# Kernel optimization log

Measured on AMD Instinct MI355X. Metric: run time of the kernel, lower is better.

Reference implementation:

```python
import jax, jax.numpy as jnp
import numpy as np

B, T, H, V = 256, 256, 512, 32000
L = 3  # stacked LSTM layers


def setup_inputs() -> dict:
    key = jax.random.key(0)
    ks = jax.random.split(key, 12)
    s = 0.05
    n = lambda k, shp: (jax.random.normal(k, shp, jnp.float32) * s)
    return {
        "text_1": jax.random.randint(ks[0], (B, T), 0, V, dtype=jnp.int32),
        "text_2": jax.random.randint(ks[1], (B, T), 0, V, dtype=jnp.int32),
        "text_3": jax.random.randint(ks[2], (B, T), 0, V, dtype=jnp.int32),
        "emb": n(ks[3], (V, H)),
        "Wx": n(ks[4], (L, H, 4 * H)),
        "Wh": n(ks[5], (L, H, 4 * H)),
        "b": jnp.zeros((L, 4 * H), jnp.float32),
        "g1": jnp.ones((3 * H,), jnp.float32), "beta1": jnp.zeros((3 * H,), jnp.float32),
        "W1": n(ks[6], (3 * H, 2 * H)), "bd1": jnp.zeros((2 * H,), jnp.float32),
        "g2": jnp.ones((2 * H,), jnp.float32), "beta2": jnp.zeros((2 * H,), jnp.float32),
        "W2": n(ks[7], (2 * H, H // 5)), "bd2": jnp.zeros((H // 5,), jnp.float32),
        "g3": jnp.ones((H // 5,), jnp.float32), "beta3": jnp.zeros((H // 5,), jnp.float32),
        "W3": n(ks[8], (H // 5, 4)), "bd3": jnp.zeros((4,), jnp.float32),
    }


def _lstm_stack(tokens, emb, Wx, Wh, b):
    # tokens: [B, T] int -> last hidden of top layer [B, H]
    x = emb[tokens]                      # [B, T, H]
    x = jnp.transpose(x, (1, 0, 2))      # [T, B, H] (scan over time)
    bsz, h = x.shape[1], Wh.shape[1]
    for l in range(Wx.shape[0]):
        Wx_l, Wh_l, b_l = Wx[l], Wh[l], b[l]
        def step(carry, xt):
            hprev, cprev = carry
            gates = xt @ Wx_l + hprev @ Wh_l + b_l      # [B, 4H]
            i, f, g, o = jnp.split(gates, 4, axis=-1)
            c = jax.nn.sigmoid(f) * cprev + jax.nn.sigmoid(i) * jnp.tanh(g)
            hnew = jax.nn.sigmoid(o) * jnp.tanh(c)
            return (hnew, c), hnew
        init = (jnp.zeros((bsz, h), x.dtype), jnp.zeros((bsz, h), x.dtype))
        _, x = jax.lax.scan(step, init, x)
    return x[-1]                          # rnn_output[:, -1, :]


def _bn(x, gamma, beta, eps=1e-3):
    m = jnp.mean(x, axis=0)
    v = jnp.var(x, axis=0)
    return gamma * (x - m) * jax.lax.rsqrt(v + eps) + beta


def reference(text_1, text_2, text_3, emb, Wx, Wh, b,
              g1, beta1, W1, bd1, g2, beta2, W2, bd2, g3, beta3, W3, bd3):
    r1 = _lstm_stack(text_1, emb, Wx, Wh, b)
    r2 = _lstm_stack(text_2, emb, Wx, Wh, b)
    r3 = _lstm_stack(text_3, emb, Wx, Wh, b)
    r = jnp.concatenate([r1, r2, r3], axis=1)   # [B, 3H]
    r = _bn(r, g1, beta1)
    r = jax.nn.selu(r @ W1 + bd1)
    r = _bn(r, g2, beta2)
    r = jax.nn.selu(r @ W2 + bd2)
    r = _bn(r, g3, beta3)
    return r @ W3 + bd3                          # [B, 4] logits
```

## Files before the change

kernel.cpp:

```cpp
#include <hip/hip_runtime.h>
#include <hip/hip_bf16.h>
#include <hip/hip_cooperative_groups.h>

namespace cg = cooperative_groups;

typedef __attribute__((ext_vector_type(8))) short short8;
typedef __attribute__((ext_vector_type(4))) float floatx4;

namespace {
constexpr int kB1 = 256;
constexpr int kT  = 256;
constexpr int kH  = 512;
constexpr int kL  = 3;
constexpr int kK  = 1024;
constexpr int kN  = 2048;
constexpr int kGrid = 576;
constexpr size_t kHB = (size_t)768 * kH;

constexpr size_t WREP_OFF   = 0;
constexpr size_t WREP_BYTES = (size_t)kL * kK * kN * 2;
constexpr size_t BREP_OFF   = WREP_OFF + WREP_BYTES;
constexpr size_t BREP_BYTES = (size_t)kL * kN * 4;
constexpr size_t HBUF_OFF   = BREP_OFF + BREP_BYTES;
constexpr size_t HBUF_BYTES = (size_t)kL * 2 * kHB * 2;
constexpr size_t CBUF_OFF   = HBUF_OFF + HBUF_BYTES;
constexpr size_t CBUF_BYTES = (size_t)kL * kHB * 4;
constexpr size_t BNA_OFF    = CBUF_OFF + CBUF_BYTES;
constexpr size_t BNC_OFF    = BNA_OFF + 1536 * 4;
constexpr size_t Z1_OFF     = BNC_OFF + 1536 * 4;
constexpr size_t Z2_OFF     = Z1_OFF + (size_t)256 * 1024 * 4;
constexpr size_t FLAG_OFF   = Z2_OFF + (size_t)256 * 102 * 4;
}

__device__ __forceinline__ float ldf(const void* p, size_t idx, int isf32) {
  if (isf32) return ((const float*)p)[idx];
  return __bfloat162float(((const __hip_bfloat16*)p)[idx]);
}

__device__ __forceinline__ short f2bs(float x) {
  union { __hip_bfloat16 h; short s; } u;
  u.h = __float2bfloat16(x);
  return u.s;
}

__device__ __forceinline__ void sync_lds() {
  asm volatile("s_waitcnt lgkmcnt(0)\n\ts_barrier" ::: "memory");
}

__device__ __forceinline__ float fast_tanh(float x) {
  float e = __expf(2.f * x);
  return __fdividef(e - 1.f, e + 1.f);
}
__device__ __forceinline__ float fast_sigmoid(float x) {
  return __fdividef(1.f, 1.f + __expf(-x));
}

__global__ void detect_kernel(const unsigned* __restrict__ g1, int* __restrict__ flag) {
  if (threadIdx.x == 0 && blockIdx.x == 0)
    *flag = (g1[0] == 0x3F800000u) ? 1 : 0;
}

__device__ __forceinline__ void repack_body(
    int start, int stride,
    const void* __restrict__ Wx, const void* __restrict__ Wh,
    const void* __restrict__ bias, int isf32,
    __hip_bfloat16* __restrict__ Wrep, float* __restrict__ brep) {
  for (int idx = start; idx < kL * kK * kN; idx += stride) {
    int j  = idx & 7;
    int n2 = (idx >> 3) & (kN - 1);
    int kg = (idx >> 14) & 127;
    int l  = idx >> 21;
    int k  = kg * 8 + j;
    int ntile = n2 >> 7, c = n2 & 127, g = c >> 5, ul = c & 31;
    int u = ntile * 32 + ul;
    int col = g * 512 + u;
    float v;
    if (k < kH) v = ldf(Wx, ((size_t)l * kH + k) * kN + col, isf32);
    else        v = ldf(Wh, ((size_t)l * kH + (k - kH)) * kN + col, isf32);
    Wrep[idx] = __float2bfloat16(v);
    if (kg == 0 && j == 0) brep[l * kN + n2] = ldf(bias, (size_t)l * kN + col, isf32);
  }
}

__global__ __launch_bounds__(256) void repack_kernel(
    const void* __restrict__ Wx, const void* __restrict__ Wh,
    const void* __restrict__ bias, const int* __restrict__ flagp,
    __hip_bfloat16* __restrict__ Wrep, float* __restrict__ brep) {
  repack_body(blockIdx.x * 256 + threadIdx.x, gridDim.x * 256, Wx, Wh, bias, *flagp,
              Wrep, brep);
}

__device__ __forceinline__ void lstm_step(
    int l, int mt, int nt, int t, int isf32,
    const __hip_bfloat16* __restrict__ WB, float bv0, float bv1,
    __hip_bfloat16* __restrict__ hbuf, float* __restrict__ cl,
    const void* __restrict__ emb, const int* __restrict__ txt,
    char* smem) {
  const int tid = threadIdx.x;
  const int lane = tid & 63;
  const int lm = lane & 15, lq = lane >> 4;
  const int arow = tid >> 2;
  const int kc   = tid & 3;
  const int row_g = mt * 64 + arow;
  const int n0w = nt * 128 + (tid >> 6) * 32;

  const void* xsrc;  bool xf32 = false;
  if (l == 0) {
    int tok = txt[t];
    if (isf32) { xsrc = (const void*)((const float*)emb + (size_t)tok * kH); xf32 = true; }
    else         xsrc = (const void*)((const __hip_bfloat16*)emb + (size_t)tok * kH);
  } else {
    const __hip_bfloat16* hIn = hbuf + ((size_t)(l - 1) * 2 + (t & 1)) * kHB;
    xsrc = (const void*)(hIn + (size_t)row_g * kH);
  }
  const __hip_bfloat16* hrow = nullptr;
  if (t > 0) {
    const __hip_bfloat16* hPrev = hbuf + ((size_t)l * 2 + ((t & 1) ^ 1)) * kHB;
    hrow = hPrev + (size_t)row_g * kH;
  }

  const int e_uu = tid & 31;
  const int e_r0 = tid >> 5;

  char* const buf0 = smem;
  char* const buf1 = smem + 16384;
  const int abase = ((arow >> 4) * 256 + kc * 16 + (arow & 15)) * 16;

  short8 av[4];
  short8 bf[4][2];

  auto loadA = [&](int sl) {
    if ((sl >= 4) && (t == 0)) {
      short8 vz = {0, 0, 0, 0, 0, 0, 0, 0};
#pragma unroll
      for (int jj = 0; jj < 4; jj++) av[jj] = vz;
    } else if (sl < 4 && xf32) {
      const float* sf = (const float*)xsrc + sl * 128;
#pragma unroll
      for (int jj = 0; jj < 4; jj++) {
        const float* q = sf + kc * 8 + jj * 32;
        float4 lo = *(const float4*)q;
        float4 hi = *(const float4*)(q + 4);
        short8 v;
        v[0] = f2bs(lo.x); v[1] = f2bs(lo.y); v[2] = f2bs(lo.z); v[3] = f2bs(lo.w);
        v[4] = f2bs(hi.x); v[5] = f2bs(hi.y); v[6] = f2bs(hi.z); v[7] = f2bs(hi.w);
        av[jj] = v;
      }
    } else {
      const __hip_bfloat16* src = (sl < 4)
          ? ((const __hip_bfloat16*)xsrc + sl * 128)
          : (hrow + (sl - 4) * 128);
#pragma unroll
      for (int jj = 0; jj < 4; jj++)
        av[jj] = *(const short8*)(src + kc * 8 + jj * 32);
    }
  };
  auto writeA = [&](char* b) {
#pragma unroll
    for (int jj = 0; jj < 4; jj++)
      *(short8*)(b + abase + jj * 1024) = av[jj];
  };
  auto loadBfrag = [&](int sl, int kk) {
#pragma unroll
    for (int nf = 0; nf < 2; nf++) {
      size_t kg = (size_t)(sl * 16 + kk * 4 + lq);
      bf[kk][nf] = *(const short8*)(WB + (kg * kN + (n0w + nf * 16 + lm)) * 8);
    }
  };

  loadA(0);
#pragma unroll
  for (int kk = 0; kk < 4; kk++) loadBfrag(0, kk);
  writeA(buf0);
  loadA(1);
  float cold[8];
  if (t > 0) {
#pragma unroll
    for (int ii = 0; ii < 8; ii++) {
      int rowf = e_r0 + 8 * ii;
      cold[ii] = cl[(size_t)(mt * 64 + rowf) * kH + nt * 32 + e_uu];
    }
  } else {
#pragma unroll
    for (int ii = 0; ii < 8; ii++) cold[ii] = 0.f;
  }
  sync_lds();

  floatx4 zf = {0.f, 0.f, 0.f, 0.f};
  floatx4 acc[4][2];
#pragma unroll
  for (int a = 0; a < 4; a++)
#pragma unroll
    for (int b = 0; b < 2; b++) acc[a][b] = zf;

#pragma unroll 1
  for (int sl = 0; sl < 8; sl++) {
    char* const cur = (sl & 1) ? buf1 : buf0;
    char* const nxt = (sl & 1) ? buf0 : buf1;
    if (sl < 7) writeA(nxt);
    if (sl < 6) loadA(sl + 2);
#pragma unroll
    for (int kk = 0; kk < 4; kk++) {
      short8 afrag[4];
#pragma unroll
      for (int mf = 0; mf < 4; mf++)
        afrag[mf] = *(const short8*)(cur + (mf * 4 + kk) * 1024 + lane * 16);
#pragma unroll
      for (int mf = 0; mf < 4; mf++)
#pragma unroll
        for (int nf = 0; nf < 2; nf++)
          acc[mf][nf] = __builtin_amdgcn_mfma_f32_16x16x32_bf16(
              afrag[mf], bf[kk][nf], acc[mf][nf], 0, 0, 0);
      if (sl < 7) loadBfrag(sl + 1, kk);
    }
    sync_lds();
  }

#pragma unroll
  for (int mf = 0; mf < 4; mf++)
#pragma unroll
    for (int r = 0; r < 4; r++) {
      acc[mf][0][r] += bv0;
      acc[mf][1][r] += bv1;
    }

  float* gl = (float*)smem;
  {
    const int wv = tid >> 6;
#pragma unroll
    for (int mf = 0; mf < 4; mf++)
#pragma unroll
      for (int nf = 0; nf < 2; nf++)
#pragma unroll
        for (int r = 0; r < 4; r++) {
          int rowf = mf * 16 + lq * 4 + r;
          int uu   = nf * 16 + lm;
          gl[((size_t)wv * 64 + rowf) * 34 + uu] = acc[mf][nf][r];
        }
  }
  sync_lds();

  __hip_bfloat16* hout = hbuf + ((size_t)l * 2 + (t & 1)) * kHB;
#pragma unroll
  for (int ii = 0; ii < 8; ii++) {
    int rowf = e_r0 + 8 * ii;
    int uu = e_uu;
    float gi = fminf(fmaxf(gl[(0 * 64 + rowf) * 34 + uu], -40.f), 40.f);
    float gf = fminf(fmaxf(gl[(1 * 64 + rowf) * 34 + uu], -40.f), 40.f);
    float gG = fminf(fmaxf(gl[(2 * 64 + rowf) * 34 + uu], -40.f), 40.f);
    float go = fminf(fmaxf(gl[(3 * 64 + rowf) * 34 + uu], -40.f), 40.f);
    size_t off = (size_t)(mt * 64 + rowf) * kH + nt * 32 + uu;
    float cn = fast_sigmoid(gf) * cold[ii] + fast_sigmoid(gi) * fast_tanh(gG);
    float hn = fast_sigmoid(go) * fast_tanh(cn);
    cl[off] = cn;
    hout[off] = __float2bfloat16(hn);
  }
  sync_lds();
}

__global__ __launch_bounds__(256, 3) void persist_kernel(
    const void* __restrict__ Wx, const void* __restrict__ Wh,
    const void* __restrict__ bias, const int* __restrict__ flagp,
    __hip_bfloat16* __restrict__ Wrep, float* __restrict__ brep,
    __hip_bfloat16* __restrict__ hbuf, float* __restrict__ cbuf,
    const void* __restrict__ emb,
    const int* __restrict__ t1, const int* __restrict__ t2, const int* __restrict__ t3) {
  cg::grid_group gg = cg::this_grid();
  __shared__ __align__(16) char smem[34816];

  const int bid = blockIdx.x;
  const int tid = threadIdx.x;
  const int isf32 = *flagp;

  repack_body(bid * 256 + tid, kGrid * 256, Wx, Wh, bias, isf32, Wrep, brep);
  gg.sync();

  const int l  = bid / 192;
  const int rr = bid % 192;
  const int nt = rr & 15;
  const int mt = rr >> 4;
  const __hip_bfloat16* const WB = Wrep + (size_t)l * kK * kN;
  float* const cl = cbuf + (size_t)l * kHB;
  const int n0w = nt * 128 + (tid >> 6) * 32;
  const int lm = tid & 15;
  const float bv0 = brep[l * kN + n0w + lm];
  const float bv1 = brep[l * kN + n0w + 16 + lm];

  const int* txt = nullptr;
  if (l == 0) {
    int row_g = mt * 64 + (tid >> 2);
    int i = row_g >> 8;
    txt = (i == 0) ? t1 : (i == 1) ? t2 : t3;
    txt += (row_g & 255) * kT;
  }

  for (int s = 0; s < kT + kL - 1; s++) {
    const int t = s - l;
    if (t >= 0 && t < kT)
      lstm_step(l, mt, nt, t, isf32, WB, bv0, bv1, hbuf, cl, emb, txt, smem);
    gg.sync();
  }
}

__global__ __launch_bounds__(256, 3) void step_kernel(
    int s,
    const __hip_bfloat16* __restrict__ Wrep, const float* __restrict__ brep,
    __hip_bfloat16* __restrict__ hbuf, float* __restrict__ cbuf,
    const void* __restrict__ emb, const int* __restrict__ flagp,
    const int* __restrict__ t1, const int* __restrict__ t2, const int* __restrict__ t3) {
  __shared__ __align__(16) char smem[34816];
  const int bid = blockIdx.x;
  const int l  = bid / 192;
  const int rr = bid % 192;
  const int nt = rr & 15;
  const int mt = rr >> 4;
  const int t = s - l;
  if (t < 0 || t >= kT) return;
  const int isf32 = *flagp;
  const int tid = threadIdx.x;
  const __hip_bfloat16* WB = Wrep + (size_t)l * kK * kN;
  float* cl = cbuf + (size_t)l * kHB;
  const int n0w = nt * 128 + (tid >> 6) * 32;
  const int lm = tid & 15;
  const float bv0 = brep[l * kN + n0w + lm];
  const float bv1 = brep[l * kN + n0w + 16 + lm];
  const int* txt = nullptr;
  if (l == 0) {
    int row_g = mt * 64 + (tid >> 2);
    int i = row_g >> 8;
    txt = (i == 0) ? t1 : (i == 1) ? t2 : t3;
    txt += (row_g & 255) * kT;
  }
  lstm_step(l, mt, nt, t, isf32, WB, bv0, bv1, hbuf, cl, emb, txt, smem);
}

__global__ __launch_bounds__(256) void stats_kernel(
    int ncols, int mode, const void* __restrict__ src,
    const void* __restrict__ gamma, const void* __restrict__ beta,
    const int* __restrict__ flagp, float* __restrict__ bn_a, float* __restrict__ bn_c) {
  int isf32 = *flagp;
  int col = blockIdx.x * 256 + threadIdx.x;
  if (col >= ncols) return;
  float sum = 0.f, ss = 0.f;
  for (int b = 0; b < kB1; b++) {
    float v;
    if (mode == 0) {
      const __hip_bfloat16* h = (const __hip_bfloat16*)src;
      v = __bfloat162float(h[((size_t)((col >> 9) * kB1 + b)) * kH + (col & 511)]);
    } else {
      v = ((const float*)src)[(size_t)b * ncols + col];
    }
    v = fmaxf(-1e15f, fminf(v, 1e15f));
    sum += v; ss += v * v;
  }
  float mean = sum * (1.f / kB1);
  float var  = ss * (1.f / kB1) - mean * mean;
  float a = ldf(gamma, col, isf32) * rsqrtf(var + 1e-3f);
  bn_a[col] = a;
  bn_c[col] = ldf(beta, col, isf32) - mean * a;
}

__global__ __launch_bounds__(256) void headgemm_kernel(
    int Kd, int Nd, int mode, const void* __restrict__ Asrc,
    const float* __restrict__ bn_a, const float* __restrict__ bn_c,
    const void* __restrict__ W, const void* __restrict__ bias,
    const int* __restrict__ flagp, float* __restrict__ out, int do_selu) {
  __shared__ float As[32][65];
  __shared__ float Bs[32][65];
  int isf32 = *flagp;
  int tid = threadIdx.x;
  int bx = blockIdx.x, by = blockIdx.y;
  int tx = tid & 15, ty = tid >> 4;
  float acc[4][4] = {};
  int am = tid & 63, ak = tid >> 6;
  int bk = tid >> 3, bn8 = (tid & 7) * 8;
  for (int ks = 0; ks < Kd; ks += 32) {
    __syncthreads();
    for (int jj = 0; jj < 8; jj++) {
      int kl = ak * 8 + jj;
      int kg = ks + kl;
      int mg = by * 64 + am;
      float v;
      if (mode == 0) {
        const __hip_bfloat16* h = (const __hip_bfloat16*)Asrc;
        v = __bfloat162float(h[((size_t)((kg >> 9) * kB1 + mg)) * kH + (kg & 511)]);
      } else {
        v = ((const float*)Asrc)[(size_t)mg * Kd + kg];
      }
      As[kl][am] = v * bn_a[kg] + bn_c[kg];
    }
    for (int e = 0; e < 8; e++) {
      int col = bx * 64 + bn8 + e;
      Bs[bk][bn8 + e] = (col < Nd) ? ldf(W, (size_t)(ks + bk) * Nd + col, isf32) : 0.f;
    }
    __syncthreads();
    for (int k = 0; k < 32; k++) {
      float ar[4], br[4];
#pragma unroll
      for (int i = 0; i < 4; i++) ar[i] = As[k][ty * 4 + i];
#pragma unroll
      for (int j = 0; j < 4; j++) br[j] = Bs[k][tx * 4 + j];
#pragma unroll
      for (int i = 0; i < 4; i++)
#pragma unroll
        for (int j = 0; j < 4; j++) acc[i][j] += ar[i] * br[j];
    }
  }
  for (int i = 0; i < 4; i++) {
    int row = by * 64 + ty * 4 + i;
    for (int j = 0; j < 4; j++) {
      int col = bx * 64 + tx * 4 + j;
      if (col < Nd) {
        float y = acc[i][j] + ldf(bias, col, isf32);
        if (do_selu)
          y = (y > 0.f) ? 1.0507009873554805f * y
                        : 1.0507009873554805f * 1.6732632423543772f * (__expf(y) - 1.f);
        out[(size_t)row * Nd + col] = y;
      }
    }
  }
}

__global__ __launch_bounds__(256) void final_kernel(
    const float* __restrict__ z2, const float* __restrict__ bn_a, const float* __restrict__ bn_c,
    const void* __restrict__ W3, const void* __restrict__ bd3,
    const int* __restrict__ flagp, void* __restrict__ out) {
  int isf32 = *flagp;
  int b = threadIdx.x;
  float acc[4] = {0.f, 0.f, 0.f, 0.f};
  for (int j = 0; j < 102; j++) {
    float y = z2[b * 102 + j] * bn_a[j] + bn_c[j];
#pragma unroll
    for (int g = 0; g < 4; g++) acc[g] += y * ldf(W3, j * 4 + g, isf32);
  }
#pragma unroll
  for (int g = 0; g < 4; g++) {
    float y = acc[g] + ldf(bd3, g, isf32);
    if (isf32) ((float*)out)[b * 4 + g] = y;
    else ((__hip_bfloat16*)out)[b * 4 + g] = __float2bfloat16(y);
  }
}

extern "C" void kernel_launch(void* const* d_in, const int* in_sizes, int n_in,
                              void* d_out, int out_size, void* d_ws, size_t ws_size,
                              hipStream_t stream) {
  const int* t1 = (const int*)d_in[0];
  const int* t2 = (const int*)d_in[1];
  const int* t3 = (const int*)d_in[2];
  const void* emb = d_in[3];
  const void* Wx  = d_in[4];
  const void* Wh  = d_in[5];
  const void* bb  = d_in[6];
  const void* g1  = d_in[7];
  const void* be1 = d_in[8];
  const void* W1  = d_in[9];
  const void* bd1 = d_in[10];
  const void* g2  = d_in[11];
  const void* be2 = d_in[12];
  const void* W2  = d_in[13];
  const void* bd2 = d_in[14];
  const void* g3  = d_in[15];
  const void* be3 = d_in[16];
  const void* W3  = d_in[17];
  const void* bd3 = d_in[18];

  char* ws = (char*)d_ws;
  __hip_bfloat16* Wrep = (__hip_bfloat16*)(ws + WREP_OFF);
  float* brep = (float*)(ws + BREP_OFF);
  __hip_bfloat16* hbuf = (__hip_bfloat16*)(ws + HBUF_OFF);
  float* cbuf = (float*)(ws + CBUF_OFF);
  float* bn_a = (float*)(ws + BNA_OFF);
  float* bn_c = (float*)(ws + BNC_OFF);
  float* z1 = (float*)(ws + Z1_OFF);
  float* z2 = (float*)(ws + Z2_OFF);
  int* flag = (int*)(ws + FLAG_OFF);

  detect_kernel<<<1, 64, 0, stream>>>((const unsigned*)g1, flag);

  bool coop_ok = false;
  {
    int numCU = 0, maxBlk = 0;
    int dev = 0;
    if (hipGetDevice(&dev) == hipSuccess &&
        hipDeviceGetAttribute(&numCU, hipDeviceAttributeMultiprocessorCount, dev) == hipSuccess &&
        hipOccupancyMaxActiveBlocksPerMultiprocessor(&maxBlk, (const void*)persist_kernel,
                                                     256, 0) == hipSuccess) {
      if ((long)maxBlk * numCU >= kGrid) {
        void* args[] = {(void*)&Wx, (void*)&Wh, (void*)&bb, (void*)&flag,
                        (void*)&Wrep, (void*)&brep, (void*)&hbuf, (void*)&cbuf,
                        (void*)&emb, (void*)&t1, (void*)&t2, (void*)&t3};
        hipError_t err = hipLaunchCooperativeKernel((const void*)persist_kernel,
                                                    dim3(kGrid), dim3(256), args, 0, stream);
        if (err == hipSuccess) coop_ok = true;
        else (void)hipGetLastError();
      }
    } else {
      (void)hipGetLastError();
    }
  }
  if (!coop_ok) {
    repack_kernel<<<(kL * kK * kN) / 256, 256, 0, stream>>>(Wx, Wh, bb, flag, Wrep, brep);
    for (int s = 0; s < kT + kL - 1; s++)
      step_kernel<<<kGrid, 256, 0, stream>>>(s, Wrep, brep, hbuf, cbuf, emb, flag, t1, t2, t3);
  }

  const __hip_bfloat16* hTop = hbuf + (2 * 2 + 1) * kHB;
  stats_kernel<<<6, 256, 0, stream>>>(1536, 0, hTop, g1, be1, flag, bn_a, bn_c);
  headgemm_kernel<<<dim3(16, 4), 256, 0, stream>>>(1536, 1024, 0, hTop, bn_a, bn_c, W1, bd1, flag, z1, 1);
  stats_kernel<<<4, 256, 0, stream>>>(1024, 1, z1, g2, be2, flag, bn_a, bn_c);
  headgemm_kernel<<<dim3(2, 4), 256, 0, stream>>>(1024, 102, 1, z1, bn_a, bn_c, W2, bd2, flag, z2, 1);
  stats_kernel<<<1, 256, 0, stream>>>(102, 1, z2, g3, be3, flag, bn_a, bn_c);
  final_kernel<<<1, 256, 0, stream>>>(z2, bn_a, bn_c, W3, bd3, flag, (void*)d_out);
}
```

Before: 6.522 ms.

## Replace grid-wide sync with per-row-tile atomic barriers and XCD-aware tile mapping

Replaces the cooperative-groups grid.sync after each timestep with custom atomic barriers scoped to the 48 blocks that share an M row-tile across all layers and N tiles. Blocks claim work slots through per-XCD atomic counters so that N tiles land on a chosen XCD, which is meant to improve L2 locality of the weight slices. The aim is to cut the cost of 258 full-grid barriers down to smaller group barriers. The trailing LDS sync in the step is dropped and the sync counters are zeroed in the detect kernel. The correctness risk lies in the cross-layer dependencies between groups and in the memory ordering of the hand-written spin barrier.

```diff
diff --git a/kernel.cpp b/kernel.cpp
--- a/kernel.cpp
+++ b/kernel.cpp
@@ -1,8 +1,5 @@
 #include <hip/hip_runtime.h>
 #include <hip/hip_bf16.h>
-#include <hip/hip_cooperative_groups.h>
-
-namespace cg = cooperative_groups;
 
 typedef __attribute__((ext_vector_type(8))) short short8;
 typedef __attribute__((ext_vector_type(4))) float floatx4;
@@ -29,7 +26,8 @@
 constexpr size_t BNC_OFF    = BNA_OFF + 1536 * 4;
 constexpr size_t Z1_OFF     = BNC_OFF + 1536 * 4;
 constexpr size_t Z2_OFF     = Z1_OFF + (size_t)256 * 1024 * 4;
-constexpr size_t FLAG_OFF   = Z2_OFF + (size_t)256 * 102 * 4;
+constexpr size_t SYNC_OFF   = Z2_OFF + (size_t)256 * 102 * 4;
+constexpr int kSyncUints = 32 * 14;
 }
 
 __device__ __forceinline__ float ldf(const void* p, size_t idx, int isf32) {
@@ -47,6 +45,25 @@
   asm volatile("s_waitcnt lgkmcnt(0)\n\ts_barrier" ::: "memory");
 }
 
+__device__ __forceinline__ void gbar(unsigned* line, unsigned target, unsigned want) {
+  __syncthreads();
+  if (threadIdx.x == 0) {
+    __threadfence();
+    unsigned old = __hip_atomic_fetch_add(&line[0], 1u, __ATOMIC_ACQ_REL,
+                                          __HIP_MEMORY_SCOPE_AGENT);
+    if (old == target - 1) {
+      __hip_atomic_store(&line[0], 0u, __ATOMIC_RELAXED, __HIP_MEMORY_SCOPE_AGENT);
+      __hip_atomic_store(&line[1], want, __ATOMIC_RELEASE, __HIP_MEMORY_SCOPE_AGENT);
+    } else {
+      while (__hip_atomic_load(&line[1], __ATOMIC_ACQUIRE,
+                               __HIP_MEMORY_SCOPE_AGENT) < want)
+        __builtin_amdgcn_s_sleep(1);
+    }
+    __threadfence();
+  }
+  __syncthreads();
+}
+
 __device__ __forceinline__ float fast_tanh(float x) {
   float e = __expf(2.f * x);
   return __fdividef(e - 1.f, e + 1.f);
@@ -55,9 +72,10 @@
   return __fdividef(1.f, 1.f + __expf(-x));
 }
 
-__global__ void detect_kernel(const unsigned* __restrict__ g1, int* __restrict__ flag) {
-  if (threadIdx.x == 0 && blockIdx.x == 0)
-    *flag = (g1[0] == 0x3F800000u) ? 1 : 0;
+__global__ void detect_kernel(const unsigned* __restrict__ g1, unsigned* __restrict__ sync) {
+  int i = threadIdx.x;
+  for (int j = i; j < kSyncUints; j += 256) sync[j] = 0u;
+  if (i == 0) sync[0] = (g1[0] == 0x3F800000u) ? 1u : 0u;
 }
 
 __device__ __forceinline__ void repack_body(
@@ -255,30 +273,48 @@
     cl[off] = cn;
     hout[off] = __float2bfloat16(hn);
   }
-  sync_lds();
 }
 
 __global__ __launch_bounds__(256, 3) void persist_kernel(
     const void* __restrict__ Wx, const void* __restrict__ Wh,
-    const void* __restrict__ bias, const int* __restrict__ flagp,
+    const void* __restrict__ bias, unsigned* __restrict__ sync,
     __hip_bfloat16* __restrict__ Wrep, float* __restrict__ brep,
     __hip_bfloat16* __restrict__ hbuf, float* __restrict__ cbuf,
     const void* __restrict__ emb,
     const int* __restrict__ t1, const int* __restrict__ t2, const int* __restrict__ t3) {
-  cg::grid_group gg = cg::this_grid();
   __shared__ __align__(16) char smem[34816];
+  __shared__ int s_tuple;
 
   const int bid = blockIdx.x;
   const int tid = threadIdx.x;
-  const int isf32 = *flagp;
+  const int isf32 = (int)sync[0];
+
+  if (tid == 0) {
+    unsigned xcd;
+    asm volatile("s_getreg_b32 %0, hwreg(20, 0, 4)" : "=s"(xcd));
+    xcd &= 7u;
+    int slot = 0;
+    for (int off = 0; off < 8; off++) {
+      unsigned x = (xcd + off) & 7u;
+      unsigned idx = __hip_atomic_fetch_add(&sync[1 + x], 1u, __ATOMIC_RELAXED,
+                                            __HIP_MEMORY_SCOPE_AGENT);
+      if (idx < 72u) { slot = (int)(x * 72u + idx); break; }
+    }
+    s_tuple = slot;
+  }
 
   repack_body(bid * 256 + tid, kGrid * 256, Wx, Wh, bias, isf32, Wrep, brep);
-  gg.sync();
-
-  const int l  = bid / 192;
-  const int rr = bid % 192;
-  const int nt = rr & 15;
-  const int mt = rr >> 4;
+  __syncthreads();
+
+  const int slot = s_tuple;
+  const int x = slot / 72, i = slot % 72;
+  const int l = i / 24;
+  const int rem = i % 24;
+  const int mt = rem % 12;
+  const int nt = x + 8 * (rem / 12);
+
+  gbar(sync + 32 * 13, kGrid, 1u);
+
   const __hip_bfloat16* const WB = Wrep + (size_t)l * kK * kN;
   float* const cl = cbuf + (size_t)l * kHB;
   const int n0w = nt * 128 + (tid >> 6) * 32;
@@ -289,16 +325,18 @@
   const int* txt = nullptr;
   if (l == 0) {
     int row_g = mt * 64 + (tid >> 2);
-    int i = row_g >> 8;
-    txt = (i == 0) ? t1 : (i == 1) ? t2 : t3;
+    int ti = row_g >> 8;
+    txt = (ti == 0) ? t1 : (ti == 1) ? t2 : t3;
     txt += (row_g & 255) * kT;
   }
 
+  unsigned* const mline = sync + 32 * (1 + mt);
   for (int s = 0; s < kT + kL - 1; s++) {
     const int t = s - l;
     if (t >= 0 && t < kT)
       lstm_step(l, mt, nt, t, isf32, WB, bv0, bv1, hbuf, cl, emb, txt, smem);
-    gg.sync();
+    if (s < kT + kL - 2)
+      gbar(mline, 48u, (unsigned)(s + 1));
   }
 }
 
@@ -327,8 +365,8 @@
   const int* txt = nullptr;
   if (l == 0) {
     int row_g = mt * 64 + (tid >> 2);
-    int i = row_g >> 8;
-    txt = (i == 0) ? t1 : (i == 1) ? t2 : t3;
+    int ti = row_g >> 8;
+    txt = (ti == 0) ? t1 : (ti == 1) ? t2 : t3;
     txt += (row_g & 255) * kT;
   }
   lstm_step(l, mt, nt, t, isf32, WB, bv0, bv1, hbuf, cl, emb, txt, smem);
@@ -473,9 +511,10 @@
   float* bn_c = (float*)(ws + BNC_OFF);
   float* z1 = (float*)(ws + Z1_OFF);
   float* z2 = (float*)(ws + Z2_OFF);
-  int* flag = (int*)(ws + FLAG_OFF);
-
-  detect_kernel<<<1, 64, 0, stream>>>((const unsigned*)g1, flag);
+  unsigned* sync = (unsigned*)(ws + SYNC_OFF);
+  const int* flag = (const int*)sync;
+
+  detect_kernel<<<1, 256, 0, stream>>>((const unsigned*)g1, sync);
 
   bool coop_ok = false;
   {
@@ -486,7 +525,7 @@
         hipOccupancyMaxActiveBlocksPerMultiprocessor(&maxBlk, (const void*)persist_kernel,
                                                      256, 0) == hipSuccess) {
       if ((long)maxBlk * numCU >= kGrid) {
-        void* args[] = {(void*)&Wx, (void*)&Wh, (void*)&bb, (void*)&flag,
+        void* args[] = {(void*)&Wx, (void*)&Wh, (void*)&bb, (void*)&sync,
                         (void*)&Wrep, (void*)&brep, (void*)&hbuf, (void*)&cbuf,
                         (void*)&emb, (void*)&t1, (void*)&t2, (void*)&t3};
         hipError_t err = hipLaunchCooperativeKernel((const void*)persist_kernel,
```

Measured after the change: 6.390 ms. 2.0% less time.
